# Optimization experiments

Measured on AMD Instinct MI355X. Metric: run time of the kernel, lower is better.

The kernel has to match this reference:

```python
import jax, jax.numpy as jnp
import numpy as np


def entmax15(z):
    """Exact 1.5-entmax along the last axis (Peters & Martins 2019, sort-based)."""
    z = z / 2.0
    z = z - jnp.max(z, axis=-1, keepdims=True)
    zs = -jnp.sort(-z, axis=-1)  # descending sort
    K = z.shape[-1]
    k = jnp.arange(1, K + 1, dtype=z.dtype)
    mean = jnp.cumsum(zs, axis=-1) / k
    mean_sq = jnp.cumsum(zs * zs, axis=-1) / k
    ss = k * (mean_sq - mean * mean)
    delta = (1.0 - ss) / k
    tau = mean - jnp.sqrt(jnp.clip(delta, 0.0))
    support = jnp.sum((tau <= zs).astype(jnp.int32), axis=-1, keepdims=True)
    tau_star = jnp.take_along_axis(tau, support - 1, axis=-1)
    p = jnp.clip(z - tau_star, 0.0)
    return p * p


def setup_inputs() -> dict:
    key = jax.random.key(0)
    k1, k2, k3 = jax.random.split(key, 3)
    N, D, P = 65536, 512, 256
    x = jax.random.normal(k1, (N, D), dtype=jnp.float32)
    prototypes = jax.random.normal(k2, (P, D), dtype=jnp.float32)
    adj_logits = jax.random.normal(k3, (P, P), dtype=jnp.float32) * 0.01
    gate_logits = jnp.zeros((P,), dtype=jnp.float32)
    gate_temp_raw = jnp.array([-2.0], dtype=jnp.float32)
    return {"x": x, "prototypes": prototypes, "adj_logits": adj_logits,
            "gate_logits": gate_logits, "gate_temp_raw": gate_temp_raw}


def reference(x, prototypes, adj_logits, gate_logits, gate_temp_raw):
    # gate temperature in (0.001, 1.0)
    gate_temp = jax.nn.sigmoid(gate_temp_raw) * (1.0 - 0.001) + 0.001
    gate = jax.nn.softmax(gate_logits / gate_temp)[None, :]  # [1, P]
    sq = (jnp.sum(x * x, axis=-1, keepdims=True)
          - 2.0 * (x @ prototypes.T)
          + jnp.sum(prototypes * prototypes, axis=-1)[None, :])
    dists = jnp.sqrt(jnp.clip(sq, 0.0))            # [N, P]
    weights = entmax15(-dists)                      # sparse routing [N, P]
    routed = weights @ entmax15(adj_logits)         # [N, P]
    gated = routed * gate
    gated = gated / (jnp.sum(gated, axis=-1, keepdims=True) + 1e-8)
    blended = gated @ prototypes                    # [N, D]
    return blended, gated
```

## Files before the change

kernel.cpp:

```cpp
#include <hip/hip_runtime.h>
#include <stdint.h>

using u16 = unsigned short;
typedef __attribute__((ext_vector_type(8))) short bf16x8;
typedef __attribute__((ext_vector_type(4))) float f32x4;

constexpr int D  = 512;
constexpr int P  = 256;
constexpr int BM = 64;
constexpr int WS = P + 8;

__device__ __forceinline__ u16 f2bf(float f) {
  uint32_t u = __builtin_bit_cast(uint32_t, f);
  u += 0x7fffu + ((u >> 16) & 1u);
  return (u16)(u >> 16);
}



__global__ void k_gate(const float* __restrict__ gl, const float* __restrict__ traw,
                       float* __restrict__ gate) {
  int l = threadIdx.x;
  float t = 1.f / (1.f + expf(-traw[0]));
  t = t * (1.f - 0.001f) + 0.001f;
  float v[4];
  float m = -3.4e38f;
  #pragma unroll
  for (int i = 0; i < 4; ++i) { v[i] = gl[l + i * 64] / t; m = fmaxf(m, v[i]); }
  #pragma unroll
  for (int s = 1; s < 64; s <<= 1) m = fmaxf(m, __shfl_xor(m, s));
  float sum = 0.f;
  #pragma unroll
  for (int i = 0; i < 4; ++i) { v[i] = expf(v[i] - m); sum += v[i]; }
  #pragma unroll
  for (int s = 1; s < 64; s <<= 1) sum += __shfl_xor(sum, s);
  #pragma unroll
  for (int i = 0; i < 4; ++i) gate[l + i * 64] = v[i] / sum;
}

__global__ void k_adj(const float* __restrict__ adj, const float* __restrict__ gate,
                      u16* __restrict__ egF) {
  int k = blockIdx.x, l = threadIdx.x;
  float z[4];
  float m = -3.4e38f;
  #pragma unroll
  for (int i = 0; i < 4; ++i) { z[i] = adj[(size_t)k * P + l + i * 64] * 0.5f; m = fmaxf(m, z[i]); }
  #pragma unroll
  for (int s = 1; s < 64; s <<= 1) m = fmaxf(m, __shfl_xor(m, s));
  float lo = m - 1.f, hi = m;
  for (int it = 0; it < 26; ++it) {
    float tau = 0.5f * (lo + hi), s = 0.f;
    #pragma unroll
    for (int i = 0; i < 4; ++i) { float d = z[i] - tau; s += (d > 0.f) ? d * d : 0.f; }
    #pragma unroll
    for (int sh = 1; sh < 64; sh <<= 1) s += __shfl_xor(s, sh);
    if (s >= 1.f) lo = tau; else hi = tau;
  }
  float tau = 0.5f * (lo + hi);
  int ss = k >> 5, g = (k >> 3) & 3, e = k & 7;
  #pragma unroll
  for (int i = 0; i < 4; ++i) {
    int j = l + i * 64;
    float d = z[i] - tau;
    float p = (d > 0.f) ? d * d : 0.f;
    int tt = j >> 4, lr = j & 15;
    egF[(size_t)(((ss * 16 + tt) * 64) + g * 16 + lr) * 8 + e] = f2bf(p * gate[j]);
  }
}

__global__ void k_proto(const float* __restrict__ proto, u16* __restrict__ pbF,
                        u16* __restrict__ ptF, float* __restrict__ pnorm) {
  int p = blockIdx.x, t = threadIdx.x;
  float s = 0.f;
  int ssp = (p >> 5) & 7, gp = (p >> 3) & 3, ep = p & 7;
  int ttp = p >> 4, lrp = p & 15;
  for (int d = t; d < D; d += 256) {
    float v = proto[(size_t)p * D + d];
    s += v * v;
    u16 u = f2bf(v);
    {
      int ss = d >> 5, g = (d >> 3) & 3, e = d & 7;
      pbF[(size_t)(((ss * 16 + ttp) * 64) + g * 16 + lrp) * 8 + e] = u;
    }
    {
      int hf = d >> 8, tt = (d >> 4) & 15, lr = d & 15;
      ptF[(size_t)(((((hf * 8 + ssp) * 16) + tt) * 64) + gp * 16 + lr) * 8 + ep] = u;
    }
  }
  #pragma unroll
  for (int sh = 1; sh < 64; sh <<= 1) s += __shfl_xor(s, sh);
  __shared__ float red[4];
  if ((t & 63) == 0) red[t >> 6] = s;
  __syncthreads();
  if (t == 0) pnorm[p] = red[0] + red[1] + red[2] + red[3];
}


__global__ __launch_bounds__(256, 4)
void k_main(const float* __restrict__ x, const u16* __restrict__ pbF,
            const u16* __restrict__ ptF, const u16* __restrict__ egF,
            const float* __restrict__ pnorm,
            float* __restrict__ out_blend, float* __restrict__ out_gated) {
  __shared__ __align__(16) u16 wbuf[BM][WS];

  int tid  = threadIdx.x;
  int brow = blockIdx.x * BM;

  int l    = tid & 63;
  int wv   = tid >> 6;
  int r0   = wv * 16;
  int lrow = l & 15;
  int lk   = (l >> 4) * 8;
  int lr4  = (l >> 4) * 4;

  float pn[16];
  #pragma unroll
  for (int c = 0; c < 16; ++c) pn[c] = pnorm[c * 16 + lrow];

  f32x4 acc[16];
  #pragma unroll
  for (int c = 0; c < 16; ++c) acc[c] = {0.f, 0.f, 0.f, 0.f};

  const float* xrow = x + (size_t)(brow + r0 + lrow) * D + lk;
  const u16*   pbB  = pbF + (size_t)l * 8;
  float ssq = 0.f;

  float4 v0 = *(const float4*)(xrow);
  float4 v1 = *(const float4*)(xrow + 4);
  #pragma unroll 1
  for (int s = 0; s < 16; ++s) {
    float4 c0 = v0, c1 = v1;
    if (s < 15) {
      v0 = *(const float4*)(xrow + s * 32 + 32);
      v1 = *(const float4*)(xrow + s * 32 + 36);
    }
    ssq += c0.x * c0.x + c0.y * c0.y + c0.z * c0.z + c0.w * c0.w;
    ssq += c1.x * c1.x + c1.y * c1.y + c1.z * c1.z + c1.w * c1.w;
    union { bf16x8 v; uint32_t u[4]; } a;
    a.u[0] = (uint32_t)f2bf(c0.x) | ((uint32_t)f2bf(c0.y) << 16);
    a.u[1] = (uint32_t)f2bf(c0.z) | ((uint32_t)f2bf(c0.w) << 16);
    a.u[2] = (uint32_t)f2bf(c1.x) | ((uint32_t)f2bf(c1.y) << 16);
    a.u[3] = (uint32_t)f2bf(c1.z) | ((uint32_t)f2bf(c1.w) << 16);
    #pragma unroll
    for (int c = 0; c < 16; ++c) {
      bf16x8 b = *(const bf16x8*)(pbB + (size_t)(s * 16 + c) * 512);
      acc[c] = __builtin_amdgcn_mfma_f32_16x16x32_bf16(a.v, b, acc[c], 0, 0, 0);
    }
  }

  ssq += __shfl_xor(ssq, 16);
  ssq += __shfl_xor(ssq, 32);
  float xnj[4];
  #pragma unroll
  for (int j = 0; j < 4; ++j) xnj[j] = __shfl(ssq, lr4 + j);

  #pragma unroll
  for (int c = 0; c < 16; ++c) {
    #pragma unroll
    for (int j = 0; j < 4; ++j) {
      float sq = xnj[j] - 2.f * acc[c][j] + pn[c];
      acc[c][j] = -0.5f * sqrtf(fmaxf(sq, 0.f));
    }
  }

  float mj[4] = {-3.4e38f, -3.4e38f, -3.4e38f, -3.4e38f};
  #pragma unroll
  for (int c = 0; c < 16; ++c) {
    #pragma unroll
    for (int j = 0; j < 4; ++j) mj[j] = fmaxf(mj[j], acc[c][j]);
  }
  #pragma unroll
  for (int j = 0; j < 4; ++j) {
    mj[j] = fmaxf(mj[j], __shfl_xor(mj[j], 1));
    mj[j] = fmaxf(mj[j], __shfl_xor(mj[j], 2));
    mj[j] = fmaxf(mj[j], __shfl_xor(mj[j], 4));
    mj[j] = fmaxf(mj[j], __shfl_xor(mj[j], 8));
  }
  float lo[4], hi[4];
  #pragma unroll
  for (int j = 0; j < 4; ++j) { lo[j] = mj[j] - 1.f; hi[j] = mj[j]; }

  for (int it = 0; it < 18; ++it) {
    float tau[4], s[4];
    #pragma unroll
    for (int j = 0; j < 4; ++j) { tau[j] = 0.5f * (lo[j] + hi[j]); s[j] = 0.f; }
    #pragma unroll
    for (int c = 0; c < 16; ++c) {
      #pragma unroll
      for (int j = 0; j < 4; ++j) {
        float d = fmaxf(acc[c][j] - tau[j], 0.f);
        s[j] = fmaf(d, d, s[j]);
      }
    }
    #pragma unroll
    for (int j = 0; j < 4; ++j) {
      s[j] += __shfl_xor(s[j], 1);
      s[j] += __shfl_xor(s[j], 2);
      s[j] += __shfl_xor(s[j], 4);
      s[j] += __shfl_xor(s[j], 8);
      bool ge = (s[j] >= 1.f);
      lo[j] = ge ? tau[j] : lo[j];
      hi[j] = ge ? hi[j] : tau[j];
    }
  }

  {
    float tau[4];
    #pragma unroll
    for (int j = 0; j < 4; ++j) tau[j] = 0.5f * (lo[j] + hi[j]);
    #pragma unroll
    for (int c = 0; c < 16; ++c) {
      #pragma unroll
      for (int j = 0; j < 4; ++j) {
        float d = fmaxf(acc[c][j] - tau[j], 0.f);
        wbuf[r0 + lr4 + j][c * 16 + lrow] = f2bf(d * d);
      }
    }
  }

  f32x4 acc2[16];
  #pragma unroll
  for (int c = 0; c < 16; ++c) acc2[c] = {0.f, 0.f, 0.f, 0.f};

  const u16* egB = egF + (size_t)l * 8;
  #pragma unroll 1
  for (int s = 0; s < 8; ++s) {
    bf16x8 a = *(const bf16x8*)&wbuf[r0 + lrow][s * 32 + lk];
    #pragma unroll
    for (int c = 0; c < 16; ++c) {
      bf16x8 b = *(const bf16x8*)(egB + (size_t)(s * 16 + c) * 512);
      acc2[c] = __builtin_amdgcn_mfma_f32_16x16x32_bf16(a, b, acc2[c], 0, 0, 0);
    }
  }

  float part[4] = {0.f, 0.f, 0.f, 0.f};
  #pragma unroll
  for (int c = 0; c < 16; ++c) {
    #pragma unroll
    for (int j = 0; j < 4; ++j) part[j] += acc2[c][j];
  }
  #pragma unroll
  for (int j = 0; j < 4; ++j) {
    part[j] += __shfl_xor(part[j], 1);
    part[j] += __shfl_xor(part[j], 2);
    part[j] += __shfl_xor(part[j], 4);
    part[j] += __shfl_xor(part[j], 8);
    part[j] = 1.f / (part[j] + 1e-8f);
  }

  #pragma unroll
  for (int c = 0; c < 16; ++c) {
    int col = c * 16 + lrow;
    #pragma unroll
    for (int j = 0; j < 4; ++j) {
      int row = r0 + lr4 + j;
      float g = acc2[c][j] * part[j];
      out_gated[(size_t)(brow + row) * P + col] = g;
      wbuf[row][col] = f2bf(g);
    }
  }

  #pragma unroll 1
  for (int half = 0; half < 2; ++half) {
    f32x4 acc3[16];
    #pragma unroll
    for (int c = 0; c < 16; ++c) acc3[c] = {0.f, 0.f, 0.f, 0.f};
    const u16* ptB = ptF + (size_t)half * 8 * 16 * 512 + (size_t)l * 8;
    #pragma unroll 1
    for (int s = 0; s < 8; ++s) {
      bf16x8 a = *(const bf16x8*)&wbuf[r0 + lrow][s * 32 + lk];
      #pragma unroll
      for (int c = 0; c < 16; ++c) {
        bf16x8 b = *(const bf16x8*)(ptB + (size_t)(s * 16 + c) * 512);
        acc3[c] = __builtin_amdgcn_mfma_f32_16x16x32_bf16(a, b, acc3[c], 0, 0, 0);
      }
    }
    #pragma unroll
    for (int c = 0; c < 16; ++c) {
      int dcol = half * 256 + c * 16 + lrow;
      #pragma unroll
      for (int j = 0; j < 4; ++j) {
        int row = r0 + lr4 + j;
        out_blend[(size_t)(brow + row) * D + dcol] = acc3[c][j];
      }
    }
  }
}


extern "C" void kernel_launch(void* const* d_in, const int* in_sizes, int n_in,
                              void* d_out, int out_size, void* d_ws, size_t ws_size,
                              hipStream_t stream) {
  const float* x     = (const float*)d_in[0];
  const float* proto = (const float*)d_in[1];
  const float* adj   = (const float*)d_in[2];
  const float* gl    = (const float*)d_in[3];
  const float* traw  = (const float*)d_in[4];
  int N = in_sizes[0] / D;

  u16*   pbF   = (u16*)d_ws;
  u16*   ptF   = pbF + (size_t)P * D;
  u16*   egF   = ptF + (size_t)D * P;
  float* pnorm = (float*)(egF + (size_t)P * P);
  float* gate  = pnorm + P;

  float* out_blend = (float*)d_out;
  float* out_gated = out_blend + (size_t)N * D;

  k_gate<<<1, 64, 0, stream>>>(gl, traw, gate);
  k_proto<<<P, 256, 0, stream>>>(proto, pbF, ptF, pnorm);
  k_adj<<<P, 64, 0, stream>>>(adj, gate, egF);
  k_main<<<N / BM, 256, 0, stream>>>(x, pbF, ptF, egF, pnorm, out_blend, out_gated);
}
```

Baseline: 421.0 us.

## Process two 16-row tiles per wave so each B-fragment load feeds two MFMAs

```diff
diff --git a/kernel.cpp b/kernel.cpp
--- a/kernel.cpp
+++ b/kernel.cpp
@@ -7,7 +7,7 @@
 
 constexpr int D  = 512;
 constexpr int P  = 256;
-constexpr int BM = 64;
+constexpr int BM = 128;
 constexpr int WS = P + 8;
 
 __device__ __forceinline__ u16 f2bf(float f) {
@@ -71,32 +71,34 @@
 __global__ void k_proto(const float* __restrict__ proto, u16* __restrict__ pbF,
                         u16* __restrict__ ptF, float* __restrict__ pnorm) {
   int p = blockIdx.x, t = threadIdx.x;
-  float s = 0.f;
+  int ttp = p >> 4, lrp = p & 15;
+  if (t < 64) {
+    int ss = t >> 2, g = t & 3;
+    int d0 = ss * 32 + g * 8;
+    float4 va = *(const float4*)(proto + (size_t)p * D + d0);
+    float4 vb = *(const float4*)(proto + (size_t)p * D + d0 + 4);
+    union { u16 h[8]; uint4 q; } pk;
+    pk.h[0] = f2bf(va.x); pk.h[1] = f2bf(va.y); pk.h[2] = f2bf(va.z); pk.h[3] = f2bf(va.w);
+    pk.h[4] = f2bf(vb.x); pk.h[5] = f2bf(vb.y); pk.h[6] = f2bf(vb.z); pk.h[7] = f2bf(vb.w);
+    *(uint4*)&pbF[(size_t)(((ss * 16 + ttp) * 64) + g * 16 + lrp) * 8] = pk.q;
+    float s = va.x * va.x + va.y * va.y + va.z * va.z + va.w * va.w
+            + vb.x * vb.x + vb.y * vb.y + vb.z * vb.z + vb.w * vb.w;
+    #pragma unroll
+    for (int sh = 1; sh < 64; sh <<= 1) s += __shfl_xor(s, sh);
+    if (t == 0) pnorm[p] = s;
+  }
   int ssp = (p >> 5) & 7, gp = (p >> 3) & 3, ep = p & 7;
-  int ttp = p >> 4, lrp = p & 15;
-  for (int d = t; d < D; d += 256) {
+  #pragma unroll
+  for (int i = 0; i < 2; ++i) {
+    int d = t + i * 256;
     float v = proto[(size_t)p * D + d];
-    s += v * v;
-    u16 u = f2bf(v);
-    {
-      int ss = d >> 5, g = (d >> 3) & 3, e = d & 7;
-      pbF[(size_t)(((ss * 16 + ttp) * 64) + g * 16 + lrp) * 8 + e] = u;
-    }
-    {
-      int hf = d >> 8, tt = (d >> 4) & 15, lr = d & 15;
-      ptF[(size_t)(((((hf * 8 + ssp) * 16) + tt) * 64) + gp * 16 + lr) * 8 + ep] = u;
-    }
-  }
-  #pragma unroll
-  for (int sh = 1; sh < 64; sh <<= 1) s += __shfl_xor(s, sh);
-  __shared__ float red[4];
-  if ((t & 63) == 0) red[t >> 6] = s;
-  __syncthreads();
-  if (t == 0) pnorm[p] = red[0] + red[1] + red[2] + red[3];
-}
-
-
-__global__ __launch_bounds__(256, 4)
+    int hf = d >> 8, tt = (d >> 4) & 15, lr = d & 15;
+    ptF[(size_t)(((((hf * 8 + ssp) * 16) + tt) * 64) + gp * 16 + lr) * 8 + ep] = f2bf(v);
+  }
+}
+
+
+__global__ __launch_bounds__(256, 2)
 void k_main(const float* __restrict__ x, const u16* __restrict__ pbF,
             const u16* __restrict__ ptF, const u16* __restrict__ egF,
             const float* __restrict__ pnorm,
@@ -108,7 +110,7 @@
 
   int l    = tid & 63;
   int wv   = tid >> 6;
-  int r0   = wv * 16;
+  int r0   = wv * 32;
   int lrow = l & 15;
   int lk   = (l >> 4) * 8;
   int lr4  = (l >> 4) * 4;
@@ -117,173 +119,249 @@
   #pragma unroll
   for (int c = 0; c < 16; ++c) pn[c] = pnorm[c * 16 + lrow];
 
-  f32x4 acc[16];
-  #pragma unroll
-  for (int c = 0; c < 16; ++c) acc[c] = {0.f, 0.f, 0.f, 0.f};
-
-  const float* xrow = x + (size_t)(brow + r0 + lrow) * D + lk;
-  const u16*   pbB  = pbF + (size_t)l * 8;
-  float ssq = 0.f;
-
-  float4 v0 = *(const float4*)(xrow);
-  float4 v1 = *(const float4*)(xrow + 4);
+  f32x4 acc[2][16];
+  #pragma unroll
+  for (int rt = 0; rt < 2; ++rt)
+    #pragma unroll
+    for (int c = 0; c < 16; ++c) acc[rt][c] = {0.f, 0.f, 0.f, 0.f};
+
+  const float* xr0 = x + (size_t)(brow + r0 + lrow) * D + lk;
+  const float* xr1 = xr0 + 16 * D;
+  const u16*   pbB = pbF + (size_t)l * 8;
+  float ssq0 = 0.f, ssq1 = 0.f;
+
+  float4 A0, A1, A2, A3, B0, B1, B2, B3;
+  A0 = *(const float4*)(xr0);      A1 = *(const float4*)(xr0 + 4);
+  A2 = *(const float4*)(xr1);      A3 = *(const float4*)(xr1 + 4);
+  B0 = *(const float4*)(xr0 + 32); B1 = *(const float4*)(xr0 + 36);
+  B2 = *(const float4*)(xr1 + 32); B3 = *(const float4*)(xr1 + 36);
+
   #pragma unroll 1
-  for (int s = 0; s < 16; ++s) {
-    float4 c0 = v0, c1 = v1;
-    if (s < 15) {
-      v0 = *(const float4*)(xrow + s * 32 + 32);
-      v1 = *(const float4*)(xrow + s * 32 + 36);
-    }
-    ssq += c0.x * c0.x + c0.y * c0.y + c0.z * c0.z + c0.w * c0.w;
-    ssq += c1.x * c1.x + c1.y * c1.y + c1.z * c1.z + c1.w * c1.w;
-    union { bf16x8 v; uint32_t u[4]; } a;
-    a.u[0] = (uint32_t)f2bf(c0.x) | ((uint32_t)f2bf(c0.y) << 16);
-    a.u[1] = (uint32_t)f2bf(c0.z) | ((uint32_t)f2bf(c0.w) << 16);
-    a.u[2] = (uint32_t)f2bf(c1.x) | ((uint32_t)f2bf(c1.y) << 16);
-    a.u[3] = (uint32_t)f2bf(c1.z) | ((uint32_t)f2bf(c1.w) << 16);
-    #pragma unroll
-    for (int c = 0; c < 16; ++c) {
-      bf16x8 b = *(const bf16x8*)(pbB + (size_t)(s * 16 + c) * 512);
-      acc[c] = __builtin_amdgcn_mfma_f32_16x16x32_bf16(a.v, b, acc[c], 0, 0, 0);
-    }
-  }
-
-  ssq += __shfl_xor(ssq, 16);
-  ssq += __shfl_xor(ssq, 32);
-  float xnj[4];
-  #pragma unroll
-  for (int j = 0; j < 4; ++j) xnj[j] = __shfl(ssq, lr4 + j);
-
-  #pragma unroll
-  for (int c = 0; c < 16; ++c) {
+  for (int s = 0; s < 16; s += 2) {
+    {
+      ssq0 += A0.x*A0.x + A0.y*A0.y + A0.z*A0.z + A0.w*A0.w
+            + A1.x*A1.x + A1.y*A1.y + A1.z*A1.z + A1.w*A1.w;
+      ssq1 += A2.x*A2.x + A2.y*A2.y + A2.z*A2.z + A2.w*A2.w
+            + A3.x*A3.x + A3.y*A3.y + A3.z*A3.z + A3.w*A3.w;
+      union { bf16x8 v; uint32_t u[4]; } fa0, fa1;
+      fa0.u[0] = (uint32_t)f2bf(A0.x) | ((uint32_t)f2bf(A0.y) << 16);
+      fa0.u[1] = (uint32_t)f2bf(A0.z) | ((uint32_t)f2bf(A0.w) << 16);
+      fa0.u[2] = (uint32_t)f2bf(A1.x) | ((uint32_t)f2bf(A1.y) << 16);
+      fa0.u[3] = (uint32_t)f2bf(A1.z) | ((uint32_t)f2bf(A1.w) << 16);
+      fa1.u[0] = (uint32_t)f2bf(A2.x) | ((uint32_t)f2bf(A2.y) << 16);
+      fa1.u[1] = (uint32_t)f2bf(A2.z) | ((uint32_t)f2bf(A2.w) << 16);
+      fa1.u[2] = (uint32_t)f2bf(A3.x) | ((uint32_t)f2bf(A3.y) << 16);
+      fa1.u[3] = (uint32_t)f2bf(A3.z) | ((uint32_t)f2bf(A3.w) << 16);
+      if (s + 2 < 16) {
+        A0 = *(const float4*)(xr0 + (s + 2) * 32);
+        A1 = *(const float4*)(xr0 + (s + 2) * 32 + 4);
+        A2 = *(const float4*)(xr1 + (s + 2) * 32);
+        A3 = *(const float4*)(xr1 + (s + 2) * 32 + 4);
+      }
+      #pragma unroll
+      for (int c = 0; c < 16; ++c) {
+        bf16x8 b = *(const bf16x8*)(pbB + (size_t)(s * 16 + c) * 512);
+        acc[0][c] = __builtin_amdgcn_mfma_f32_16x16x32_bf16(fa0.v, b, acc[0][c], 0, 0, 0);
+        acc[1][c] = __builtin_amdgcn_mfma_f32_16x16x32_bf16(fa1.v, b, acc[1][c], 0, 0, 0);
+      }
+    }
+    {
+      ssq0 += B0.x*B0.x + B0.y*B0.y + B0.z*B0.z + B0.w*B0.w
+            + B1.x*B1.x + B1.y*B1.y + B1.z*B1.z + B1.w*B1.w;
+      ssq1 += B2.x*B2.x + B2.y*B2.y + B2.z*B2.z + B2.w*B2.w
+            + B3.x*B3.x + B3.y*B3.y + B3.z*B3.z + B3.w*B3.w;
+      union { bf16x8 v; uint32_t u[4]; } fb0, fb1;
+      fb0.u[0] = (uint32_t)f2bf(B0.x) | ((uint32_t)f2bf(B0.y) << 16);
+      fb0.u[1] = (uint32_t)f2bf(B0.z) | ((uint32_t)f2bf(B0.w) << 16);
+      fb0.u[2] = (uint32_t)f2bf(B1.x) | ((uint32_t)f2bf(B1.y) << 16);
+      fb0.u[3] = (uint32_t)f2bf(B1.z) | ((uint32_t)f2bf(B1.w) << 16);
+      fb1.u[0] = (uint32_t)f2bf(B2.x) | ((uint32_t)f2bf(B2.y) << 16);
+      fb1.u[1] = (uint32_t)f2bf(B2.z) | ((uint32_t)f2bf(B2.w) << 16);
+      fb1.u[2] = (uint32_t)f2bf(B3.x) | ((uint32_t)f2bf(B3.y) << 16);
+      fb1.u[3] = (uint32_t)f2bf(B3.z) | ((uint32_t)f2bf(B3.w) << 16);
+      if (s + 3 < 16) {
+        B0 = *(const float4*)(xr0 + (s + 3) * 32);
+        B1 = *(const float4*)(xr0 + (s + 3) * 32 + 4);
+        B2 = *(const float4*)(xr1 + (s + 3) * 32);
+        B3 = *(const float4*)(xr1 + (s + 3) * 32 + 4);
+      }
+      #pragma unroll
+      for (int c = 0; c < 16; ++c) {
+        bf16x8 b = *(const bf16x8*)(pbB + (size_t)((s + 1) * 16 + c) * 512);
+        acc[0][c] = __builtin_amdgcn_mfma_f32_16x16x32_bf16(fb0.v, b, acc[0][c], 0, 0, 0);
+        acc[1][c] = __builtin_amdgcn_mfma_f32_16x16x32_bf16(fb1.v, b, acc[1][c], 0, 0, 0);
+      }
+    }
+  }
+
+  ssq0 += __shfl_xor(ssq0, 16); ssq0 += __shfl_xor(ssq0, 32);
+  ssq1 += __shfl_xor(ssq1, 16); ssq1 += __shfl_xor(ssq1, 32);
+  float xnj[2][4];
+  #pragma unroll
+  for (int j = 0; j < 4; ++j) {
+    xnj[0][j] = __shfl(ssq0, lr4 + j);
+    xnj[1][j] = __shfl(ssq1, lr4 + j);
+  }
+
+  #pragma unroll
+  for (int rt = 0; rt < 2; ++rt)
+    #pragma unroll
+    for (int c = 0; c < 16; ++c)
+      #pragma unroll
+      for (int j = 0; j < 4; ++j) {
+        float sq = xnj[rt][j] - 2.f * acc[rt][c][j] + pn[c];
+        acc[rt][c][j] = -0.5f * sqrtf(fmaxf(sq, 0.f));
+      }
+
+  float mj[2][4] = {{-3.4e38f,-3.4e38f,-3.4e38f,-3.4e38f},{-3.4e38f,-3.4e38f,-3.4e38f,-3.4e38f}};
+  #pragma unroll
+  for (int rt = 0; rt < 2; ++rt)
+    #pragma unroll
+    for (int c = 0; c < 16; ++c)
+      #pragma unroll
+      for (int j = 0; j < 4; ++j) mj[rt][j] = fmaxf(mj[rt][j], acc[rt][c][j]);
+  #pragma unroll
+  for (int rt = 0; rt < 2; ++rt)
     #pragma unroll
     for (int j = 0; j < 4; ++j) {
-      float sq = xnj[j] - 2.f * acc[c][j] + pn[c];
-      acc[c][j] = -0.5f * sqrtf(fmaxf(sq, 0.f));
-    }
-  }
-
-  float mj[4] = {-3.4e38f, -3.4e38f, -3.4e38f, -3.4e38f};
-  #pragma unroll
-  for (int c = 0; c < 16; ++c) {
-    #pragma unroll
-    for (int j = 0; j < 4; ++j) mj[j] = fmaxf(mj[j], acc[c][j]);
-  }
-  #pragma unroll
-  for (int j = 0; j < 4; ++j) {
-    mj[j] = fmaxf(mj[j], __shfl_xor(mj[j], 1));
-    mj[j] = fmaxf(mj[j], __shfl_xor(mj[j], 2));
-    mj[j] = fmaxf(mj[j], __shfl_xor(mj[j], 4));
-    mj[j] = fmaxf(mj[j], __shfl_xor(mj[j], 8));
-  }
-  float lo[4], hi[4];
-  #pragma unroll
-  for (int j = 0; j < 4; ++j) { lo[j] = mj[j] - 1.f; hi[j] = mj[j]; }
+      mj[rt][j] = fmaxf(mj[rt][j], __shfl_xor(mj[rt][j], 1));
+      mj[rt][j] = fmaxf(mj[rt][j], __shfl_xor(mj[rt][j], 2));
+      mj[rt][j] = fmaxf(mj[rt][j], __shfl_xor(mj[rt][j], 4));
+      mj[rt][j] = fmaxf(mj[rt][j], __shfl_xor(mj[rt][j], 8));
+    }
+  float lo[2][4], hi[2][4];
+  #pragma unroll
+  for (int rt = 0; rt < 2; ++rt)
+    #pragma unroll
+    for (int j = 0; j < 4; ++j) { lo[rt][j] = mj[rt][j] - 1.f; hi[rt][j] = mj[rt][j]; }
 
   for (int it = 0; it < 18; ++it) {
-    float tau[4], s[4];
-    #pragma unroll
-    for (int j = 0; j < 4; ++j) { tau[j] = 0.5f * (lo[j] + hi[j]); s[j] = 0.f; }
-    #pragma unroll
-    for (int c = 0; c < 16; ++c) {
+    float tau[2][4], s[2][4];
+    #pragma unroll
+    for (int rt = 0; rt < 2; ++rt)
+      #pragma unroll
+      for (int j = 0; j < 4; ++j) { tau[rt][j] = 0.5f * (lo[rt][j] + hi[rt][j]); s[rt][j] = 0.f; }
+    #pragma unroll
+    for (int c = 0; c < 16; ++c)
+      #pragma unroll
+      for (int rt = 0; rt < 2; ++rt)
+        #pragma unroll
+        for (int j = 0; j < 4; ++j) {
+          float d = fmaxf(acc[rt][c][j] - tau[rt][j], 0.f);
+          s[rt][j] = fmaf(d, d, s[rt][j]);
+        }
+    #pragma unroll
+    for (int rt = 0; rt < 2; ++rt)
       #pragma unroll
       for (int j = 0; j < 4; ++j) {
-        float d = fmaxf(acc[c][j] - tau[j], 0.f);
-        s[j] = fmaf(d, d, s[j]);
-      }
-    }
-    #pragma unroll
-    for (int j = 0; j < 4; ++j) {
-      s[j] += __shfl_xor(s[j], 1);
-      s[j] += __shfl_xor(s[j], 2);
-      s[j] += __shfl_xor(s[j], 4);
-      s[j] += __shfl_xor(s[j], 8);
-      bool ge = (s[j] >= 1.f);
-      lo[j] = ge ? tau[j] : lo[j];
-      hi[j] = ge ? hi[j] : tau[j];
-    }
+        s[rt][j] += __shfl_xor(s[rt][j], 1);
+        s[rt][j] += __shfl_xor(s[rt][j], 2);
+        s[rt][j] += __shfl_xor(s[rt][j], 4);
+        s[rt][j] += __shfl_xor(s[rt][j], 8);
+        bool ge = (s[rt][j] >= 1.f);
+        lo[rt][j] = ge ? tau[rt][j] : lo[rt][j];
+        hi[rt][j] = ge ? hi[rt][j] : tau[rt][j];
+      }
   }
 
   {
-    float tau[4];
-    #pragma unroll
-    for (int j = 0; j < 4; ++j) tau[j] = 0.5f * (lo[j] + hi[j]);
-    #pragma unroll
-    for (int c = 0; c < 16; ++c) {
-      #pragma unroll
-      for (int j = 0; j < 4; ++j) {
-        float d = fmaxf(acc[c][j] - tau[j], 0.f);
-        wbuf[r0 + lr4 + j][c * 16 + lrow] = f2bf(d * d);
-      }
-    }
-  }
-
-  f32x4 acc2[16];
-  #pragma unroll
-  for (int c = 0; c < 16; ++c) acc2[c] = {0.f, 0.f, 0.f, 0.f};
+    float tau[2][4];
+    #pragma unroll
+    for (int rt = 0; rt < 2; ++rt)
+      #pragma unroll
+      for (int j = 0; j < 4; ++j) tau[rt][j] = 0.5f * (lo[rt][j] + hi[rt][j]);
+    #pragma unroll
+    for (int rt = 0; rt < 2; ++rt)
+      #pragma unroll
+      for (int c = 0; c < 16; ++c)
+        #pragma unroll
+        for (int j = 0; j < 4; ++j) {
+          float d = fmaxf(acc[rt][c][j] - tau[rt][j], 0.f);
+          wbuf[r0 + rt * 16 + lr4 + j][c * 16 + lrow] = f2bf(d * d);
+        }
+  }
+
+  f32x4 acc2[2][16];
+  #pragma unroll
+  for (int rt = 0; rt < 2; ++rt)
+    #pragma unroll
+    for (int c = 0; c < 16; ++c) acc2[rt][c] = {0.f, 0.f, 0.f, 0.f};
 
   const u16* egB = egF + (size_t)l * 8;
   #pragma unroll 1
   for (int s = 0; s < 8; ++s) {
-    bf16x8 a = *(const bf16x8*)&wbuf[r0 + lrow][s * 32 + lk];
+    bf16x8 a0 = *(const bf16x8*)&wbuf[r0 + lrow][s * 32 + lk];
+    bf16x8 a1 = *(const bf16x8*)&wbuf[r0 + 16 + lrow][s * 32 + lk];
     #pragma unroll
     for (int c = 0; c < 16; ++c) {
       bf16x8 b = *(const bf16x8*)(egB + (size_t)(s * 16 + c) * 512);
-      acc2[c] = __builtin_amdgcn_mfma_f32_16x16x32_bf16(a, b, acc2[c], 0, 0, 0);
-    }
-  }
-
-  float part[4] = {0.f, 0.f, 0.f, 0.f};
-  #pragma unroll
-  for (int c = 0; c < 16; ++c) {
-    #pragma unroll
-    for (int j = 0; j < 4; ++j) part[j] += acc2[c][j];
-  }
-  #pragma unroll
-  for (int j = 0; j < 4; ++j) {
-    part[j] += __shfl_xor(part[j], 1);
-    part[j] += __shfl_xor(part[j], 2);
-    part[j] += __shfl_xor(part[j], 4);
-    part[j] += __shfl_xor(part[j], 8);
-    part[j] = 1.f / (part[j] + 1e-8f);
-  }
-
-  #pragma unroll
-  for (int c = 0; c < 16; ++c) {
-    int col = c * 16 + lrow;
+      acc2[0][c] = __builtin_amdgcn_mfma_f32_16x16x32_bf16(a0, b, acc2[0][c], 0, 0, 0);
+      acc2[1][c] = __builtin_amdgcn_mfma_f32_16x16x32_bf16(a1, b, acc2[1][c], 0, 0, 0);
+    }
+  }
+
+  float part[2][4] = {{0.f,0.f,0.f,0.f},{0.f,0.f,0.f,0.f}};
+  #pragma unroll
+  for (int rt = 0; rt < 2; ++rt)
+    #pragma unroll
+    for (int c = 0; c < 16; ++c)
+      #pragma unroll
+      for (int j = 0; j < 4; ++j) part[rt][j] += acc2[rt][c][j];
+  #pragma unroll
+  for (int rt = 0; rt < 2; ++rt)
     #pragma unroll
     for (int j = 0; j < 4; ++j) {
-      int row = r0 + lr4 + j;
-      float g = acc2[c][j] * part[j];
-      out_gated[(size_t)(brow + row) * P + col] = g;
-      wbuf[row][col] = f2bf(g);
-    }
-  }
+      part[rt][j] += __shfl_xor(part[rt][j], 1);
+      part[rt][j] += __shfl_xor(part[rt][j], 2);
+      part[rt][j] += __shfl_xor(part[rt][j], 4);
+      part[rt][j] += __shfl_xor(part[rt][j], 8);
+      part[rt][j] = 1.f / (part[rt][j] + 1e-8f);
+    }
+
+  #pragma unroll
+  for (int rt = 0; rt < 2; ++rt)
+    #pragma unroll
+    for (int c = 0; c < 16; ++c) {
+      int col = c * 16 + lrow;
+      #pragma unroll
+      for (int j = 0; j < 4; ++j) {
+        int row = r0 + rt * 16 + lr4 + j;
+        float g = acc2[rt][c][j] * part[rt][j];
+        out_gated[(size_t)(brow + row) * P + col] = g;
+        wbuf[row][col] = f2bf(g);
+      }
+    }
 
   #pragma unroll 1
   for (int half = 0; half < 2; ++half) {
-    f32x4 acc3[16];
-    #pragma unroll
-    for (int c = 0; c < 16; ++c) acc3[c] = {0.f, 0.f, 0.f, 0.f};
+    f32x4 acc3[2][16];
+    #pragma unroll
+    for (int rt = 0; rt < 2; ++rt)
+      #pragma unroll
+      for (int c = 0; c < 16; ++c) acc3[rt][c] = {0.f, 0.f, 0.f, 0.f};
     const u16* ptB = ptF + (size_t)half * 8 * 16 * 512 + (size_t)l * 8;
     #pragma unroll 1
     for (int s = 0; s < 8; ++s) {
-      bf16x8 a = *(const bf16x8*)&wbuf[r0 + lrow][s * 32 + lk];
+      bf16x8 a0 = *(const bf16x8*)&wbuf[r0 + lrow][s * 32 + lk];
+      bf16x8 a1 = *(const bf16x8*)&wbuf[r0 + 16 + lrow][s * 32 + lk];
       #pragma unroll
       for (int c = 0; c < 16; ++c) {
         bf16x8 b = *(const bf16x8*)(ptB + (size_t)(s * 16 + c) * 512);
-        acc3[c] = __builtin_amdgcn_mfma_f32_16x16x32_bf16(a, b, acc3[c], 0, 0, 0);
-      }
-    }
-    #pragma unroll
-    for (int c = 0; c < 16; ++c) {
-      int dcol = half * 256 + c * 16 + lrow;
-      #pragma unroll
-      for (int j = 0; j < 4; ++j) {
-        int row = r0 + lr4 + j;
-        out_blend[(size_t)(brow + row) * D + dcol] = acc3[c][j];
-      }
-    }
+        acc3[0][c] = __builtin_amdgcn_mfma_f32_16x16x32_bf16(a0, b, acc3[0][c], 0, 0, 0);
+        acc3[1][c] = __builtin_amdgcn_mfma_f32_16x16x32_bf16(a1, b, acc3[1][c], 0, 0, 0);
+      }
+    }
+    #pragma unroll
+    for (int rt = 0; rt < 2; ++rt)
+      #pragma unroll
+      for (int c = 0; c < 16; ++c) {
+        int dcol = half * 256 + c * 16 + lrow;
+        #pragma unroll
+        for (int j = 0; j < 4; ++j) {
+          int row = r0 + rt * 16 + lr4 + j;
+          out_blend[(size_t)(brow + row) * D + dcol] = acc3[rt][c][j];
+        }
+      }
   }
 }
 
```

Result: no change. 427.7 us (+1.6%).

## Double-buffer B-fragment register loads, swizzle LDS tile, vectorize prototype packing

Applied to the files above, without the earlier changes.

```diff
diff --git a/kernel.cpp b/kernel.cpp
--- a/kernel.cpp
+++ b/kernel.cpp
@@ -8,12 +8,27 @@
 constexpr int D  = 512;
 constexpr int P  = 256;
 constexpr int BM = 64;
-constexpr int WS = P + 8;
 
 __device__ __forceinline__ u16 f2bf(float f) {
   uint32_t u = __builtin_bit_cast(uint32_t, f);
   u += 0x7fffu + ((u >> 16) & 1u);
   return (u16)(u >> 16);
+}
+
+__device__ __forceinline__ int swz(int row, int col) {
+  return (row * 256 + col) ^ ((row & 7) << 3);
+}
+
+__device__ __forceinline__ bf16x8 pack8(const float4& a, const float4& b) {
+  union { bf16x8 v; uint32_t u[4]; } r;
+  r.u[0] = (uint32_t)f2bf(a.x) | ((uint32_t)f2bf(a.y) << 16);
+  r.u[1] = (uint32_t)f2bf(a.z) | ((uint32_t)f2bf(a.w) << 16);
+  r.u[2] = (uint32_t)f2bf(b.x) | ((uint32_t)f2bf(b.y) << 16);
+  r.u[3] = (uint32_t)f2bf(b.z) | ((uint32_t)f2bf(b.w) << 16);
+  return r.v;
+}
+__device__ __forceinline__ float dot4(const float4& v) {
+  return v.x * v.x + v.y * v.y + v.z * v.z + v.w * v.w;
 }
 
 
@@ -71,37 +86,38 @@
 __global__ void k_proto(const float* __restrict__ proto, u16* __restrict__ pbF,
                         u16* __restrict__ ptF, float* __restrict__ pnorm) {
   int p = blockIdx.x, t = threadIdx.x;
-  float s = 0.f;
+  int ttp = p >> 4, lrp = p & 15;
+  if (t < 64) {
+    int ss = t >> 2, g = t & 3;
+    int d0 = ss * 32 + g * 8;
+    float4 va = *(const float4*)(proto + (size_t)p * D + d0);
+    float4 vb = *(const float4*)(proto + (size_t)p * D + d0 + 4);
+    union { u16 h[8]; uint4 q; } pk;
+    pk.h[0] = f2bf(va.x); pk.h[1] = f2bf(va.y); pk.h[2] = f2bf(va.z); pk.h[3] = f2bf(va.w);
+    pk.h[4] = f2bf(vb.x); pk.h[5] = f2bf(vb.y); pk.h[6] = f2bf(vb.z); pk.h[7] = f2bf(vb.w);
+    *(uint4*)&pbF[(size_t)(((ss * 16 + ttp) * 64) + g * 16 + lrp) * 8] = pk.q;
+    float s = dot4(va) + dot4(vb);
+    #pragma unroll
+    for (int sh = 1; sh < 64; sh <<= 1) s += __shfl_xor(s, sh);
+    if (t == 0) pnorm[p] = s;
+  }
   int ssp = (p >> 5) & 7, gp = (p >> 3) & 3, ep = p & 7;
-  int ttp = p >> 4, lrp = p & 15;
-  for (int d = t; d < D; d += 256) {
+  #pragma unroll
+  for (int i = 0; i < 2; ++i) {
+    int d = t + i * 256;
     float v = proto[(size_t)p * D + d];
-    s += v * v;
-    u16 u = f2bf(v);
-    {
-      int ss = d >> 5, g = (d >> 3) & 3, e = d & 7;
-      pbF[(size_t)(((ss * 16 + ttp) * 64) + g * 16 + lrp) * 8 + e] = u;
-    }
-    {
-      int hf = d >> 8, tt = (d >> 4) & 15, lr = d & 15;
-      ptF[(size_t)(((((hf * 8 + ssp) * 16) + tt) * 64) + gp * 16 + lr) * 8 + ep] = u;
-    }
-  }
-  #pragma unroll
-  for (int sh = 1; sh < 64; sh <<= 1) s += __shfl_xor(s, sh);
-  __shared__ float red[4];
-  if ((t & 63) == 0) red[t >> 6] = s;
-  __syncthreads();
-  if (t == 0) pnorm[p] = red[0] + red[1] + red[2] + red[3];
-}
-
-
-__global__ __launch_bounds__(256, 4)
+    int hf = d >> 8, tt = (d >> 4) & 15, lr = d & 15;
+    ptF[(size_t)(((((hf * 8 + ssp) * 16) + tt) * 64) + gp * 16 + lr) * 8 + ep] = f2bf(v);
+  }
+}
+
+
+__global__ __launch_bounds__(256, 5)
 void k_main(const float* __restrict__ x, const u16* __restrict__ pbF,
             const u16* __restrict__ ptF, const u16* __restrict__ egF,
             const float* __restrict__ pnorm,
             float* __restrict__ out_blend, float* __restrict__ out_gated) {
-  __shared__ __align__(16) u16 wbuf[BM][WS];
+  __shared__ __align__(16) u16 wbuf[BM * P];
 
   int tid  = threadIdx.x;
   int brow = blockIdx.x * BM;
@@ -113,10 +129,6 @@
   int lk   = (l >> 4) * 8;
   int lr4  = (l >> 4) * 4;
 
-  float pn[16];
-  #pragma unroll
-  for (int c = 0; c < 16; ++c) pn[c] = pnorm[c * 16 + lrow];
-
   f32x4 acc[16];
   #pragma unroll
   for (int c = 0; c < 16; ++c) acc[c] = {0.f, 0.f, 0.f, 0.f};
@@ -125,27 +137,42 @@
   const u16*   pbB  = pbF + (size_t)l * 8;
   float ssq = 0.f;
 
-  float4 v0 = *(const float4*)(xrow);
-  float4 v1 = *(const float4*)(xrow + 4);
+  bf16x8 b0[16], b1[16];
+  #pragma unroll
+  for (int c = 0; c < 16; ++c) b0[c] = *(const bf16x8*)(pbB + (size_t)c * 512);
+
+  float4 A0 = *(const float4*)(xrow),      A1 = *(const float4*)(xrow + 4);
+  float4 B0 = *(const float4*)(xrow + 32), B1 = *(const float4*)(xrow + 36);
+
   #pragma unroll 1
-  for (int s = 0; s < 16; ++s) {
-    float4 c0 = v0, c1 = v1;
-    if (s < 15) {
-      v0 = *(const float4*)(xrow + s * 32 + 32);
-      v1 = *(const float4*)(xrow + s * 32 + 36);
-    }
-    ssq += c0.x * c0.x + c0.y * c0.y + c0.z * c0.z + c0.w * c0.w;
-    ssq += c1.x * c1.x + c1.y * c1.y + c1.z * c1.z + c1.w * c1.w;
-    union { bf16x8 v; uint32_t u[4]; } a;
-    a.u[0] = (uint32_t)f2bf(c0.x) | ((uint32_t)f2bf(c0.y) << 16);
-    a.u[1] = (uint32_t)f2bf(c0.z) | ((uint32_t)f2bf(c0.w) << 16);
-    a.u[2] = (uint32_t)f2bf(c1.x) | ((uint32_t)f2bf(c1.y) << 16);
-    a.u[3] = (uint32_t)f2bf(c1.z) | ((uint32_t)f2bf(c1.w) << 16);
-    #pragma unroll
-    for (int c = 0; c < 16; ++c) {
-      bf16x8 b = *(const bf16x8*)(pbB + (size_t)(s * 16 + c) * 512);
-      acc[c] = __builtin_amdgcn_mfma_f32_16x16x32_bf16(a.v, b, acc[c], 0, 0, 0);
-    }
+  for (int s = 0; s < 16; s += 2) {
+    #pragma unroll
+    for (int c = 0; c < 16; ++c)
+      b1[c] = *(const bf16x8*)(pbB + (size_t)((s + 1) * 16 + c) * 512);
+    ssq += dot4(A0) + dot4(A1);
+    bf16x8 fa = pack8(A0, A1);
+    if (s + 2 < 16) {
+      A0 = *(const float4*)(xrow + (s + 2) * 32);
+      A1 = *(const float4*)(xrow + (s + 2) * 32 + 4);
+    }
+    #pragma unroll
+    for (int c = 0; c < 16; ++c)
+      acc[c] = __builtin_amdgcn_mfma_f32_16x16x32_bf16(fa, b0[c], acc[c], 0, 0, 0);
+
+    if (s + 2 < 16) {
+      #pragma unroll
+      for (int c = 0; c < 16; ++c)
+        b0[c] = *(const bf16x8*)(pbB + (size_t)((s + 2) * 16 + c) * 512);
+    }
+    ssq += dot4(B0) + dot4(B1);
+    bf16x8 fb = pack8(B0, B1);
+    if (s + 3 < 16) {
+      B0 = *(const float4*)(xrow + (s + 3) * 32);
+      B1 = *(const float4*)(xrow + (s + 3) * 32 + 4);
+    }
+    #pragma unroll
+    for (int c = 0; c < 16; ++c)
+      acc[c] = __builtin_amdgcn_mfma_f32_16x16x32_bf16(fb, b1[c], acc[c], 0, 0, 0);
   }
 
   ssq += __shfl_xor(ssq, 16);
@@ -154,6 +181,10 @@
   #pragma unroll
   for (int j = 0; j < 4; ++j) xnj[j] = __shfl(ssq, lr4 + j);
 
+  float pn[16];
+  #pragma unroll
+  for (int c = 0; c < 16; ++c) pn[c] = pnorm[c * 16 + lrow];
+
   #pragma unroll
   for (int c = 0; c < 16; ++c) {
     #pragma unroll
@@ -162,6 +193,10 @@
       acc[c][j] = -0.5f * sqrtf(fmaxf(sq, 0.f));
     }
   }
+
+  const u16* egB = egF + (size_t)l * 8;
+  #pragma unroll
+  for (int c = 0; c < 16; ++c) b0[c] = *(const bf16x8*)(egB + (size_t)c * 512);
 
   float mj[4] = {-3.4e38f, -3.4e38f, -3.4e38f, -3.4e38f};
   #pragma unroll
@@ -213,7 +248,7 @@
       #pragma unroll
       for (int j = 0; j < 4; ++j) {
         float d = fmaxf(acc[c][j] - tau[j], 0.f);
-        wbuf[r0 + lr4 + j][c * 16 + lrow] = f2bf(d * d);
+        wbuf[swz(r0 + lr4 + j, c * 16 + lrow)] = f2bf(d * d);
       }
     }
   }
@@ -222,15 +257,25 @@
   #pragma unroll
   for (int c = 0; c < 16; ++c) acc2[c] = {0.f, 0.f, 0.f, 0.f};
 
-  const u16* egB = egF + (size_t)l * 8;
   #pragma unroll 1
-  for (int s = 0; s < 8; ++s) {
-    bf16x8 a = *(const bf16x8*)&wbuf[r0 + lrow][s * 32 + lk];
-    #pragma unroll
-    for (int c = 0; c < 16; ++c) {
-      bf16x8 b = *(const bf16x8*)(egB + (size_t)(s * 16 + c) * 512);
-      acc2[c] = __builtin_amdgcn_mfma_f32_16x16x32_bf16(a, b, acc2[c], 0, 0, 0);
-    }
+  for (int s = 0; s < 8; s += 2) {
+    #pragma unroll
+    for (int c = 0; c < 16; ++c)
+      b1[c] = *(const bf16x8*)(egB + (size_t)((s + 1) * 16 + c) * 512);
+    bf16x8 a0 = *(const bf16x8*)&wbuf[swz(r0 + lrow, s * 32 + lk)];
+    #pragma unroll
+    for (int c = 0; c < 16; ++c)
+      acc2[c] = __builtin_amdgcn_mfma_f32_16x16x32_bf16(a0, b0[c], acc2[c], 0, 0, 0);
+
+    if (s + 2 < 8) {
+      #pragma unroll
+      for (int c = 0; c < 16; ++c)
+        b0[c] = *(const bf16x8*)(egB + (size_t)((s + 2) * 16 + c) * 512);
+    }
+    bf16x8 a1 = *(const bf16x8*)&wbuf[swz(r0 + lrow, (s + 1) * 32 + lk)];
+    #pragma unroll
+    for (int c = 0; c < 16; ++c)
+      acc2[c] = __builtin_amdgcn_mfma_f32_16x16x32_bf16(a1, b1[c], acc2[c], 0, 0, 0);
   }
 
   float part[4] = {0.f, 0.f, 0.f, 0.f};
@@ -248,6 +293,10 @@
     part[j] = 1.f / (part[j] + 1e-8f);
   }
 
+  const u16* ptB = ptF + (size_t)l * 8;
+  #pragma unroll
+  for (int c = 0; c < 16; ++c) b0[c] = *(const bf16x8*)(ptB + (size_t)c * 512);
+
   #pragma unroll
   for (int c = 0; c < 16; ++c) {
     int col = c * 16 + lrow;
@@ -256,34 +305,70 @@
       int row = r0 + lr4 + j;
       float g = acc2[c][j] * part[j];
       out_gated[(size_t)(brow + row) * P + col] = g;
-      wbuf[row][col] = f2bf(g);
-    }
-  }
-
+      wbuf[swz(row, col)] = f2bf(g);
+    }
+  }
+
+  f32x4 acc3[16];
+  #pragma unroll
+  for (int c = 0; c < 16; ++c) acc3[c] = {0.f, 0.f, 0.f, 0.f};
   #pragma unroll 1
-  for (int half = 0; half < 2; ++half) {
-    f32x4 acc3[16];
-    #pragma unroll
-    for (int c = 0; c < 16; ++c) acc3[c] = {0.f, 0.f, 0.f, 0.f};
-    const u16* ptB = ptF + (size_t)half * 8 * 16 * 512 + (size_t)l * 8;
-    #pragma unroll 1
-    for (int s = 0; s < 8; ++s) {
-      bf16x8 a = *(const bf16x8*)&wbuf[r0 + lrow][s * 32 + lk];
-      #pragma unroll
-      for (int c = 0; c < 16; ++c) {
-        bf16x8 b = *(const bf16x8*)(ptB + (size_t)(s * 16 + c) * 512);
-        acc3[c] = __builtin_amdgcn_mfma_f32_16x16x32_bf16(a, b, acc3[c], 0, 0, 0);
-      }
-    }
-    #pragma unroll
-    for (int c = 0; c < 16; ++c) {
-      int dcol = half * 256 + c * 16 + lrow;
-      #pragma unroll
-      for (int j = 0; j < 4; ++j) {
-        int row = r0 + lr4 + j;
-        out_blend[(size_t)(brow + row) * D + dcol] = acc3[c][j];
-      }
-    }
+  for (int s = 0; s < 8; s += 2) {
+    #pragma unroll
+    for (int c = 0; c < 16; ++c)
+      b1[c] = *(const bf16x8*)(ptB + (size_t)((s + 1) * 16 + c) * 512);
+    bf16x8 a0 = *(const bf16x8*)&wbuf[swz(r0 + lrow, s * 32 + lk)];
+    #pragma unroll
+    for (int c = 0; c < 16; ++c)
+      acc3[c] = __builtin_amdgcn_mfma_f32_16x16x32_bf16(a0, b0[c], acc3[c], 0, 0, 0);
+    if (s + 2 < 8) {
+      #pragma unroll
+      for (int c = 0; c < 16; ++c)
+        b0[c] = *(const bf16x8*)(ptB + (size_t)((s + 2) * 16 + c) * 512);
+    }
+    bf16x8 a1 = *(const bf16x8*)&wbuf[swz(r0 + lrow, (s + 1) * 32 + lk)];
+    #pragma unroll
+    for (int c = 0; c < 16; ++c)
+      acc3[c] = __builtin_amdgcn_mfma_f32_16x16x32_bf16(a1, b1[c], acc3[c], 0, 0, 0);
+  }
+  #pragma unroll
+  for (int c = 0; c < 16; ++c)
+    b0[c] = *(const bf16x8*)(ptB + (size_t)(8 * 16 + c) * 512);
+  #pragma unroll
+  for (int c = 0; c < 16; ++c) {
+    int dcol = c * 16 + lrow;
+    #pragma unroll
+    for (int j = 0; j < 4; ++j)
+      out_blend[(size_t)(brow + r0 + lr4 + j) * D + dcol] = acc3[c][j];
+  }
+
+  #pragma unroll
+  for (int c = 0; c < 16; ++c) acc3[c] = {0.f, 0.f, 0.f, 0.f};
+  #pragma unroll 1
+  for (int s = 0; s < 8; s += 2) {
+    #pragma unroll
+    for (int c = 0; c < 16; ++c)
+      b1[c] = *(const bf16x8*)(ptB + (size_t)((8 + s + 1) * 16 + c) * 512);
+    bf16x8 a0 = *(const bf16x8*)&wbuf[swz(r0 + lrow, s * 32 + lk)];
+    #pragma unroll
+    for (int c = 0; c < 16; ++c)
+      acc3[c] = __builtin_amdgcn_mfma_f32_16x16x32_bf16(a0, b0[c], acc3[c], 0, 0, 0);
+    if (s + 2 < 8) {
+      #pragma unroll
+      for (int c = 0; c < 16; ++c)
+        b0[c] = *(const bf16x8*)(ptB + (size_t)((8 + s + 2) * 16 + c) * 512);
+    }
+    bf16x8 a1 = *(const bf16x8*)&wbuf[swz(r0 + lrow, (s + 1) * 32 + lk)];
+    #pragma unroll
+    for (int c = 0; c < 16; ++c)
+      acc3[c] = __builtin_amdgcn_mfma_f32_16x16x32_bf16(a1, b1[c], acc3[c], 0, 0, 0);
+  }
+  #pragma unroll
+  for (int c = 0; c < 16; ++c) {
+    int dcol = 256 + c * 16 + lrow;
+    #pragma unroll
+    for (int j = 0; j < 4; ++j)
+      out_blend[(size_t)(brow + r0 + lr4 + j) * D + dcol] = acc3[c][j];
   }
 }
 
```

Result: slower. 1.054 ms (+150.4%).
